# Optimization experiments

Hardware: AMD Instinct MI355X
Metric: run time of the kernel (lower is better)

Reference implementation:

```python
import jax, jax.numpy as jnp
import numpy as np

N_QUBITS = 16
N_LAYERS = 2
NUM_CLASSES = 10
BATCH = 256

# CNOT as (c_out, t_out, c_in, t_in)
_CNOT = np.zeros((2, 2, 2, 2), dtype=np.complex64)
_CNOT[0, 0, 0, 0] = 1; _CNOT[0, 1, 0, 1] = 1
_CNOT[1, 1, 1, 0] = 1; _CNOT[1, 0, 1, 1] = 1
CNOT = jnp.asarray(_CNOT)


def rot_matrix(phi, theta, omega):
    # PennyLane Rot = RZ(omega) @ RY(theta) @ RZ(phi)
    c, s = jnp.cos(theta / 2), jnp.sin(theta / 2)
    m00 = jnp.exp(-0.5j * (phi + omega)) * c
    m01 = -jnp.exp(0.5j * (phi - omega)) * s
    m10 = jnp.exp(-0.5j * (phi - omega)) * s
    m11 = jnp.exp(0.5j * (phi + omega)) * c
    return jnp.stack([jnp.stack([m00, m01]), jnp.stack([m10, m11])]).astype(jnp.complex64)


def apply_1q(state, U, w, n):
    # state: (B, 2**n); wire 0 = most-significant bit (PennyLane convention)
    B = state.shape[0]
    st = state.reshape(B, 2 ** w, 2, -1)
    st = jnp.einsum('oi,baic->baoc', U, st)
    return st.reshape(B, -1)


def apply_cnot(state, c, t, n):
    B = state.shape[0]
    st = state.reshape((B,) + (2,) * n)
    st = jnp.tensordot(CNOT, st, axes=[[2, 3], [c + 1, t + 1]])  # new c,t axes at front
    st = jnp.moveaxis(st, [0, 1], [c + 1, t + 1])
    return st.reshape(B, -1)


def circuit_expvals(x, q_params, n, n_layers):
    # AmplitudeEmbedding with normalize=True
    norm = jnp.sqrt(jnp.sum(x * x, axis=-1, keepdims=True))
    psi = (x / norm).astype(jnp.complex64)
    for l in range(n_layers):
        for w in range(n):
            U = rot_matrix(q_params[l, w, 0], q_params[l, w, 1], q_params[l, w, 2])
            psi = apply_1q(psi, U, w, n)
        r = (l % (n - 1)) + 1  # default StronglyEntanglingLayers ranges
        for w in range(n):
            psi = apply_cnot(psi, w, (w + r) % n, n)
    probs = psi.real ** 2 + psi.imag ** 2  # (B, 2**n)
    B = probs.shape[0]
    ev = []
    for w in range(n):
        p = probs.reshape(B, 2 ** w, 2, -1)
        ev.append(p[:, :, 0, :].sum(axis=(1, 2)) - p[:, :, 1, :].sum(axis=(1, 2)))
    return jnp.stack(ev, axis=1)  # (B, n)


def setup_inputs() -> dict:
    key = jax.random.key(0)
    k1, k2, k3, k4 = jax.random.split(key, 4)
    x = jax.random.normal(k1, (BATCH, 2 ** N_QUBITS), dtype=jnp.float32)
    q_params = jax.random.normal(k2, (N_LAYERS, N_QUBITS, 3), dtype=jnp.float32)
    lim = 1.0 / np.sqrt(N_QUBITS)
    W = jax.random.uniform(k3, (NUM_CLASSES, N_QUBITS), jnp.float32, -lim, lim)
    b = jax.random.uniform(k4, (NUM_CLASSES,), jnp.float32, -lim, lim)
    return {"x": x, "q_params": q_params, "W": W, "b": b}


def reference(x, q_params, W, b):
    feats = circuit_expvals(x, q_params, N_QUBITS, N_LAYERS)  # (B, n_qubits)
    return feats @ W.T + b
```

## Files before the change

kernel.cpp:

```cpp
#include <hip/hip_runtime.h>


#define BATCH 256
#define NCLS 10

typedef _Float16 h2 __attribute__((ext_vector_type(2)));
typedef float v2f __attribute__((ext_vector_type(2)));

#define KATTR __launch_bounds__(256, 4)

struct CircuitMeta { unsigned l1mask[16]; unsigned l1role[16]; unsigned fin[16]; };

__host__ __device__ constexpr CircuitMeta make_meta() {
  CircuitMeta m{};
  unsigned col[16] = {}, inv[16] = {};
  for (int w = 0; w < 16; ++w) { col[w] = 1u << (15 - w); inv[w] = 1u << (15 - w); }
  for (int w = 0; w < 16; ++w) { int c = w, t = (w + 1) & 15; col[c] ^= col[t]; inv[t] ^= inv[c]; }
  for (int w = 0; w < 16; ++w) { m.l1mask[w] = col[w]; m.l1role[w] = inv[w]; }
  for (int w = 0; w < 16; ++w) { int c = w, t = (w + 2) & 15; col[c] ^= col[t]; inv[t] ^= inv[c]; }
  for (int w = 0; w < 16; ++w) m.fin[w] = inv[w];
  return m;
}
constexpr CircuitMeta META = make_meta();

__host__ __device__ constexpr unsigned HASH(unsigned i) {
  return i ^ ((i >> 4) & 15u) ^ ((i >> 8) & 15u);
}

__device__ __forceinline__ h2 hfma(h2 a, h2 b, h2 c) {
  return __builtin_elementwise_fma(a, b, c);
}
__device__ __forceinline__ h2 hswp(h2 a) { return __builtin_shufflevector(a, a, 1, 0); }
__device__ __forceinline__ v2f vfma(v2f a, v2f b, v2f c) {
  return __builtin_elementwise_fma(a, b, c);
}
__device__ __forceinline__ unsigned U32(h2 a) { return __builtin_bit_cast(unsigned, a); }
__device__ __forceinline__ h2 H2(unsigned u) { return __builtin_bit_cast(h2, u); }
__device__ __forceinline__ unsigned AMPU(h2 r, h2 i, int l) {
  h2 a = l ? (h2){r.y, i.y} : (h2){r.x, i.x};
  return U32(a);
}

__device__ __forceinline__ float esel(int q, int pos, float e00, float e01,
                                      float e10, float e11) {
  int p = q ? 3 - pos : pos;
  return p == 0 ? e00 : p == 1 ? e01 : p == 2 ? e10 : e11;
}

template<int KB0,int KB1,int KB2,int KB3,int LB, unsigned MG, unsigned RG>
__device__ __forceinline__ void gateV(h2 (&Vr)[16], h2 (&Vi)[16],
                                      const float* __restrict__ g,
                                      int gi, unsigned tp) {
  constexpr unsigned cover = (1u<<KB0)|(1u<<KB1)|(1u<<KB2)|(1u<<KB3)|(1u<<LB);
  static_assert((MG & ~cover) == 0u, "gate mask not covered by stage reg bits");
  constexpr unsigned mk = ((MG>>KB0)&1u) | (((MG>>KB1)&1u)<<1)
                        | (((MG>>KB2)&1u)<<2) | (((MG>>KB3)&1u)<<3);
  constexpr int ml = (int)((MG>>LB)&1u);
  constexpr unsigned rk = ((RG>>KB0)&1u) | (((RG>>KB1)&1u)<<1)
                        | (((RG>>KB2)&1u)<<2) | (((RG>>KB3)&1u)<<3);
  constexpr int rl = (int)((RG>>LB)&1u);
  static_assert(mk != 0u || ml != 0, "empty mask");

  float u00r = g[gi*8+0], u00i = g[gi*8+1], u01r = g[gi*8+2], u01i = g[gi*8+3];
  float u10r = g[gi*8+4], u10i = g[gi*8+5], u11r = g[gi*8+6], u11i = g[gi*8+7];
  const bool s = (__popc(RG & tp) & 1) != 0;
  float e00r = s?u11r:u00r, e00i = s?u11i:u00i;
  float e01r = s?u10r:u01r, e01i = s?u10i:u01i;
  float e10r = s?u01r:u10r, e10i = s?u01i:u10i;
  float e11r = s?u00r:u11r, e11i = s?u00i:u11i;
  #define ER(q,pos) (_Float16)esel((q),(pos),e00r,e01r,e10r,e11r)
  #define EI(q,pos) (_Float16)esel((q),(pos),e00i,e01i,e10i,e11i)

  if constexpr (ml == 0) {
    static_assert((__builtin_popcount(rk & mk) & 1) == 1, "pair parity invariant");
    h2 c00r = {ER(0,0), ER(rl,0)}, c00i = {EI(0,0), EI(rl,0)};
    h2 c01r = {ER(0,1), ER(rl,1)}, c01i = {EI(0,1), EI(rl,1)};
    h2 c10r = {ER(0,2), ER(rl,2)}, c10i = {EI(0,2), EI(rl,2)};
    h2 c11r = {ER(0,3), ER(rl,3)}, c11i = {EI(0,3), EI(rl,3)};
    constexpr unsigned pivot = mk & (0u - mk);
    #pragma unroll
    for (int k0 = 0; k0 < 16; ++k0) {
      if (k0 & (int)pivot) continue;
      const int k1 = k0 ^ (int)mk;
      const bool podd = (__builtin_popcount(rk & (unsigned)k0) & 1) != 0;
      const h2 A0r = podd?c11r:c00r, A0i = podd?c11i:c00i;
      const h2 A1r = podd?c10r:c01r, A1i = podd?c10i:c01i;
      const h2 B0r = podd?c01r:c10r, B0i = podd?c01i:c10i;
      const h2 B1r = podd?c00r:c11r, B1i = podd?c00i:c11i;
      const h2 v0r = Vr[k0], v0i = Vi[k0], v1r = Vr[k1], v1i = Vi[k1];
      h2 n0r = A0r*v0r; n0r = hfma(-A0i, v0i, n0r);
      n0r = hfma(A1r, v1r, n0r); n0r = hfma(-A1i, v1i, n0r);
      h2 n0i = A0r*v0i; n0i = hfma(A0i, v0r, n0i);
      n0i = hfma(A1r, v1i, n0i); n0i = hfma(A1i, v1r, n0i);
      h2 n1r = B0r*v0r; n1r = hfma(-B0i, v0i, n1r);
      n1r = hfma(B1r, v1r, n1r); n1r = hfma(-B1i, v1i, n1r);
      h2 n1i = B0r*v0i; n1i = hfma(B0i, v0r, n1i);
      n1i = hfma(B1r, v1i, n1i); n1i = hfma(B1i, v1r, n1i);
      Vr[k0] = n0r; Vi[k0] = n0i; Vr[k1] = n1r; Vi[k1] = n1i;
    }
  } else if constexpr (mk == 0u) {
    static_assert(rl == 1, "lane-only gate requires rl==1");
    h2 CA0r = {ER(0,0), ER(1,0)}, CA0i = {EI(0,0), EI(1,0)};
    h2 CB0r = {ER(0,1), ER(1,1)}, CB0i = {EI(0,1), EI(1,1)};
    h2 CA1r = {ER(1,0), ER(0,0)}, CA1i = {EI(1,0), EI(0,0)};
    h2 CB1r = {ER(1,1), ER(0,1)}, CB1i = {EI(1,1), EI(0,1)};
    #pragma unroll
    for (int k = 0; k < 16; ++k) {
      const bool q = (__builtin_popcount(rk & (unsigned)k) & 1) != 0;
      const h2 CAr = q?CA1r:CA0r, CAi = q?CA1i:CA0i;
      const h2 CBr = q?CB1r:CB0r, CBi = q?CB1i:CB0i;
      const h2 vr = Vr[k], vi = Vi[k];
      const h2 svr = hswp(vr), svi = hswp(vi);
      h2 nr = CAr*vr; nr = hfma(-CAi, vi, nr);
      nr = hfma(CBr, svr, nr); nr = hfma(-CBi, svi, nr);
      h2 ni = CAr*vi; ni = hfma(CAi, vr, ni);
      ni = hfma(CBr, svi, ni); ni = hfma(CBi, svr, ni);
      Vr[k] = nr; Vi[k] = ni;
    }
  } else {
    constexpr int dm = __builtin_popcount(rk & mk) & 1;
    static_assert((dm ^ rl) == 1, "cross gate pair parity invariant");
    h2 CA0r = {ER(0,0), ER(rl,0)},          CA0i = {EI(0,0), EI(rl,0)};
    h2 CB0r = {ER(0,1), ER(rl,1)},          CB0i = {EI(0,1), EI(rl,1)};
    h2 CC0r = {ER(dm,0), ER(dm^rl,0)},      CC0i = {EI(dm,0), EI(dm^rl,0)};
    h2 CD0r = {ER(dm,1), ER(dm^rl,1)},      CD0i = {EI(dm,1), EI(dm^rl,1)};
    h2 CA1r = {ER(1,0), ER(1^rl,0)},        CA1i = {EI(1,0), EI(1^rl,0)};
    h2 CB1r = {ER(1,1), ER(1^rl,1)},        CB1i = {EI(1,1), EI(1^rl,1)};
    h2 CC1r = {ER(1^dm,0), ER(1^dm^rl,0)},  CC1i = {EI(1^dm,0), EI(1^dm^rl,0)};
    h2 CD1r = {ER(1^dm,1), ER(1^dm^rl,1)},  CD1i = {EI(1^dm,1), EI(1^dm^rl,1)};
    constexpr unsigned pivot = mk & (0u - mk);
    #pragma unroll
    for (int k0 = 0; k0 < 16; ++k0) {
      if (k0 & (int)pivot) continue;
      const int k1 = k0 ^ (int)mk;
      const bool q = (__builtin_popcount(rk & (unsigned)k0) & 1) != 0;
      const h2 CAr = q?CA1r:CA0r, CAi = q?CA1i:CA0i;
      const h2 CBr = q?CB1r:CB0r, CBi = q?CB1i:CB0i;
      const h2 CCr = q?CC1r:CC0r, CCi = q?CC1i:CC0i;
      const h2 CDr = q?CD1r:CD0r, CDi = q?CD1i:CD0i;
      const h2 vr = Vr[k0], vi = Vi[k0], ur = Vr[k1], ui = Vi[k1];
      const h2 sur = hswp(ur), sui = hswp(ui), svr = hswp(vr), svi = hswp(vi);
      h2 nvr = CAr*vr; nvr = hfma(-CAi, vi, nvr);
      nvr = hfma(CBr, sur, nvr); nvr = hfma(-CBi, sui, nvr);
      h2 nvi = CAr*vi; nvi = hfma(CAi, vr, nvi);
      nvi = hfma(CBr, sui, nvi); nvi = hfma(CBi, sur, nvi);
      h2 nur = CCr*ur; nur = hfma(-CCi, ui, nur);
      nur = hfma(CDr, svr, nur); nur = hfma(-CDi, svi, nur);
      h2 nui = CCr*ui; nui = hfma(CCi, ur, nui);
      nui = hfma(CDr, svi, nui); nui = hfma(CDi, svr, nui);
      Vr[k0] = nvr; Vi[k0] = nvi; Vr[k1] = nur; Vi[k1] = nui;
    }
  }
  #undef ER
  #undef EI
}

__global__ void prep_gates(const float* __restrict__ qp, float* __restrict__ g) {
  int i = threadIdx.x;
  if (i >= 32) return;
  float phi = qp[i*3+0], th = qp[i*3+1], om = qp[i*3+2];
  float cth = cosf(0.5f*th), sth = sinf(0.5f*th);
  float a = 0.5f*(phi+om), d = 0.5f*(phi-om);
  float ca = cosf(a), sa = sinf(a), cd = cosf(d), sd = sinf(d);
  g[i*8+0] =  ca*cth; g[i*8+1] = -sa*cth;
  g[i*8+2] = -cd*sth; g[i*8+3] = -sd*sth;
  g[i*8+4] =  cd*sth; g[i*8+5] = -sd*sth;
  g[i*8+6] =  ca*cth; g[i*8+7] =  sa*cth;
}

__global__ KATTR void passA(const float* __restrict__ x,
    unsigned* __restrict__ st, const float* __restrict__ g) {
  __shared__ unsigned L[8192];
  const int t = threadIdx.x;
  const int batch = blockIdx.x >> 3;
  const unsigned f = blockIdx.x & 7;
  const float* xb = x + ((size_t)batch << 16) + ((size_t)f << 13);

  h2 Vr[16], Vi[16];
  #pragma unroll
  for (int k = 0; k < 16; ++k) {
    Vr[k] = (h2){(_Float16)xb[((unsigned)k << 9) | (unsigned)t],
                 (_Float16)xb[((unsigned)k << 9) | 256u | (unsigned)t]};
    Vi[k] = (h2){(_Float16)0.f, (_Float16)0.f};
  }

  gateV<9,10,11,12,8, 0x1000u,0x1000u>(Vr, Vi, g, 3, 0u);
  gateV<9,10,11,12,8, 0x0800u,0x0800u>(Vr, Vi, g, 4, 0u);
  gateV<9,10,11,12,8, 0x0400u,0x0400u>(Vr, Vi, g, 5, 0u);
  gateV<9,10,11,12,8, 0x0200u,0x0200u>(Vr, Vi, g, 6, 0u);
  gateV<9,10,11,12,8, 0x0100u,0x0100u>(Vr, Vi, g, 7, 0u);

  {
    const unsigned wb = HASH((unsigned)t);
    #pragma unroll
    for (int k = 0; k < 16; ++k) {
      L[wb ^ HASH(((unsigned)k << 9))]        = AMPU(Vr[k], Vi[k], 0);
      L[wb ^ HASH(((unsigned)k << 9) | 256u)] = AMPU(Vr[k], Vi[k], 1);
    }
    __syncthreads();
    const unsigned rb = HASH((((unsigned)t & 0xF8u) << 5) | ((unsigned)t & 7u));
    #pragma unroll
    for (int k = 0; k < 16; ++k) {
      h2 h0 = H2(L[rb ^ HASH(((unsigned)k << 4))]);
      h2 h1 = H2(L[rb ^ HASH(((unsigned)k << 4) | 8u)]);
      Vr[k] = (h2){h0.x, h1.x};
      Vi[k] = (h2){h0.y, h1.y};
    }
  }

  gateV<4,5,6,7,3, 0x0080u,0x0080u>(Vr, Vi, g,  8, 0u);
  gateV<4,5,6,7,3, 0x0040u,0x0040u>(Vr, Vi, g,  9, 0u);
  gateV<4,5,6,7,3, 0x0020u,0x0020u>(Vr, Vi, g, 10, 0u);
  gateV<4,5,6,7,3, 0x0010u,0x0010u>(Vr, Vi, g, 11, 0u);
  gateV<4,5,6,7,3, 0x0008u,0x0008u>(Vr, Vi, g, 12, 0u);

  __syncthreads();
  {
    const unsigned wb = HASH((((unsigned)t & 0xF8u) << 5) | ((unsigned)t & 7u));
    #pragma unroll
    for (int k = 0; k < 16; ++k) {
      L[wb ^ HASH(((unsigned)k << 4))]      = AMPU(Vr[k], Vi[k], 0);
      L[wb ^ HASH(((unsigned)k << 4) | 8u)] = AMPU(Vr[k], Vi[k], 1);
    }
    __syncthreads();
    const unsigned rb = HASH((unsigned)t << 3);
    #pragma unroll
    for (int k = 0; k < 16; ++k) {
      const unsigned kv = ((unsigned)k & 7u) | (((unsigned)k & 8u) << 8);
      h2 h0 = H2(L[rb ^ HASH(kv)]);
      h2 h1 = H2(L[rb ^ HASH(kv | 4096u)]);
      Vr[k] = (h2){h0.x, h1.x};
      Vi[k] = (h2){h0.y, h1.y};
    }
  }

  gateV<0,1,2,11,12, 0x0004u,0x0004u>(Vr, Vi, g, 13, 0u);
  gateV<0,1,2,11,12, 0x0002u,0x0002u>(Vr, Vi, g, 14, 0u);
  gateV<0,1,2,11,12, 0x0001u,0x0001u>(Vr, Vi, g, 15, 0u);

  unsigned* outb = st + ((size_t)batch << 16) + ((size_t)f << 13);
  #pragma unroll
  for (int l = 0; l < 2; ++l) {
    #pragma unroll
    for (int kh = 0; kh < 2; ++kh) {
      uint4 q0, q1;
      q0.x = AMPU(Vr[kh*8+0], Vi[kh*8+0], l); q0.y = AMPU(Vr[kh*8+1], Vi[kh*8+1], l);
      q0.z = AMPU(Vr[kh*8+2], Vi[kh*8+2], l); q0.w = AMPU(Vr[kh*8+3], Vi[kh*8+3], l);
      q1.x = AMPU(Vr[kh*8+4], Vi[kh*8+4], l); q1.y = AMPU(Vr[kh*8+5], Vi[kh*8+5], l);
      q1.z = AMPU(Vr[kh*8+6], Vi[kh*8+6], l); q1.w = AMPU(Vr[kh*8+7], Vi[kh*8+7], l);
      const unsigned si = ((unsigned)l << 12) | ((unsigned)kh << 11) | ((unsigned)t << 3);
      *(uint4*)(outb + si) = q0;
      *(uint4*)(outb + si + 4) = q1;
    }
  }
}

__global__ KATTR void passB(unsigned* __restrict__ st,
    const float* __restrict__ g) {
  __shared__ unsigned L[8192];
  const int t = threadIdx.x;
  const int batch = blockIdx.x >> 3;
  const unsigned c = blockIdx.x & 7;
  unsigned* stb = st + ((size_t)batch << 16);

  const unsigned lbase = ((unsigned)t & 127u) | (((unsigned)t & 128u) << 3) | (c << 7);
  h2 Vr[16], Vi[16];
  #pragma unroll
  for (int k = 0; k < 16; ++k) {
    h2 h0 = H2(stb[((unsigned)k << 12) | lbase]);
    h2 h1 = H2(stb[((unsigned)k << 12) | 2048u | lbase]);
    Vr[k] = (h2){h0.x, h1.x};
    Vi[k] = (h2){h0.y, h1.y};
  }

  const unsigned tp1 = lbase;
  gateV<12,13,14,15,11, 0x8000u,0x8000u>(Vr, Vi, g, 0, tp1);
  gateV<12,13,14,15,11, 0x4000u,0x4000u>(Vr, Vi, g, 1, tp1);
  gateV<12,13,14,15,11, 0x2000u,0x2000u>(Vr, Vi, g, 2, tp1);
  gateV<12,13,14,15,11, META.l1mask[0], META.l1role[0]>(Vr, Vi, g, 16, tp1);
  gateV<12,13,14,15,11, META.l1mask[1], META.l1role[1]>(Vr, Vi, g, 17, tp1);
  gateV<12,13,14,15,11, META.l1mask[2], META.l1role[2]>(Vr, Vi, g, 18, tp1);
  gateV<12,13,14,15,11, META.l1mask[3], META.l1role[3]>(Vr, Vi, g, 19, tp1);

  {
    const unsigned wb = HASH((unsigned)t);
    #pragma unroll
    for (int k = 0; k < 16; ++k) {
      L[wb ^ HASH(((unsigned)k << 9))]        = AMPU(Vr[k], Vi[k], 0);
      L[wb ^ HASH(((unsigned)k << 9) | 256u)] = AMPU(Vr[k], Vi[k], 1);
    }
    __syncthreads();
    const unsigned rb = HASH((((unsigned)t & 0xF0u) << 5) | (((unsigned)t & 15u) << 1));
    #pragma unroll
    for (int k = 0; k < 16; ++k) {
      h2 h0 = H2(L[rb ^ HASH(((unsigned)k << 5))]);
      h2 h1 = H2(L[rb ^ HASH(((unsigned)k << 5) | 1u)]);
      Vr[k] = (h2){h0.x, h1.x};
      Vi[k] = (h2){h0.y, h1.y};
    }
  }

  const unsigned tp2 = (((unsigned)t & 0xF0u) << 8) | (((unsigned)t & 15u) << 1) | (c << 7);
  gateV<5,6,10,11,0, META.l1mask[4], META.l1role[4]>(Vr, Vi, g, 20, tp2);
  gateV<5,6,10,11,0, META.l1mask[9], META.l1role[9]>(Vr, Vi, g, 25, tp2);

  __syncthreads();
  {
    const unsigned wb = HASH((((unsigned)t & 0xF0u) << 5) | (((unsigned)t & 15u) << 1));
    #pragma unroll
    for (int k = 0; k < 16; ++k) {
      L[wb ^ HASH(((unsigned)k << 5))]      = AMPU(Vr[k], Vi[k], 0);
      L[wb ^ HASH(((unsigned)k << 5) | 1u)] = AMPU(Vr[k], Vi[k], 1);
    }
    __syncthreads();
    const unsigned rb = HASH((((unsigned)t & 0xFEu) << 5) | ((unsigned)t & 1u));
    #pragma unroll
    for (int k = 0; k < 16; ++k) {
      h2 h0 = H2(L[rb ^ HASH(((unsigned)k << 2))]);
      h2 h1 = H2(L[rb ^ HASH(((unsigned)k << 2) | 2u)]);
      Vr[k] = (h2){h0.x, h1.x};
      Vi[k] = (h2){h0.y, h1.y};
    }
  }

  const unsigned tp3 = (((unsigned)t & 0xFCu) << 8) | (((unsigned)t & 2u) << 5)
                     | ((unsigned)t & 1u) | (c << 7);
  gateV<2,3,4,5,1, META.l1mask[10], META.l1role[10]>(Vr, Vi, g, 26, tp3);
  gateV<2,3,4,5,1, META.l1mask[11], META.l1role[11]>(Vr, Vi, g, 27, tp3);
  gateV<2,3,4,5,1, META.l1mask[12], META.l1role[12]>(Vr, Vi, g, 28, tp3);
  gateV<2,3,4,5,1, META.l1mask[13], META.l1role[13]>(Vr, Vi, g, 29, tp3);

  __syncthreads();
  {
    const unsigned wb = HASH((((unsigned)t & 0xFEu) << 5) | ((unsigned)t & 1u));
    #pragma unroll
    for (int k = 0; k < 16; ++k) {
      L[wb ^ HASH(((unsigned)k << 2))]      = AMPU(Vr[k], Vi[k], 0);
      L[wb ^ HASH(((unsigned)k << 2) | 2u)] = AMPU(Vr[k], Vi[k], 1);
    }
    __syncthreads();
    const unsigned rb = HASH((unsigned)t << 2);
    #pragma unroll
    for (int k = 0; k < 16; ++k) {
      const unsigned kv = ((unsigned)k & 3u) | (((unsigned)k & 12u) << 9);
      h2 h0 = H2(L[rb ^ HASH(kv)]);
      h2 h1 = H2(L[rb ^ HASH(kv | 1024u)]);
      Vr[k] = (h2){h0.x, h1.x};
      Vi[k] = (h2){h0.y, h1.y};
    }
  }

  const unsigned tp4 = (((unsigned)t & 0xE0u) << 5) | (((unsigned)t & 31u) << 2) | (c << 7);
  gateV<0,1,14,15,13, META.l1mask[14], META.l1role[14]>(Vr, Vi, g, 30, tp4);
  gateV<0,1,14,15,13, META.l1mask[15], META.l1role[15]>(Vr, Vi, g, 31, tp4);

  #pragma unroll
  for (int l = 0; l < 2; ++l) {
    #pragma unroll
    for (int kh = 0; kh < 4; ++kh) {
      uint4 q;
      q.x = AMPU(Vr[kh*4+0], Vi[kh*4+0], l); q.y = AMPU(Vr[kh*4+1], Vi[kh*4+1], l);
      q.z = AMPU(Vr[kh*4+2], Vi[kh*4+2], l); q.w = AMPU(Vr[kh*4+3], Vi[kh*4+3], l);
      *(uint4*)(stb + (tp4 | ((unsigned)l << 13) | ((unsigned)kh << 14))) = q;
    }
  }
}

__global__ KATTR void passC(const unsigned* __restrict__ st,
    const float* __restrict__ g, float* __restrict__ partials) {
  __shared__ float R[4][17];
  const int t = threadIdx.x;
  const int batch = blockIdx.x >> 3;
  const unsigned f = blockIdx.x & 7;
  const unsigned* stb = st + ((size_t)batch << 16);

  const unsigned cbase = (f << 13) | (((unsigned)t & 192u) << 5) | ((unsigned)t & 63u);
  h2 Vr[16], Vi[16];
  #pragma unroll
  for (int k = 0; k < 16; ++k) {
    h2 h0 = H2(stb[cbase | ((unsigned)k << 7)]);
    h2 h1 = H2(stb[cbase | ((unsigned)k << 7) | 64u]);
    Vr[k] = (h2){h0.x, h1.x};
    Vi[k] = (h2){h0.y, h1.y};
  }

  gateV<7,8,9,10,6, META.l1mask[5], META.l1role[5]>(Vr, Vi, g, 21, cbase);
  gateV<7,8,9,10,6, META.l1mask[6], META.l1role[6]>(Vr, Vi, g, 22, cbase);
  gateV<7,8,9,10,6, META.l1mask[7], META.l1role[7]>(Vr, Vi, g, 23, cbase);
  gateV<7,8,9,10,6, META.l1mask[8], META.l1role[8]>(Vr, Vi, g, 24, cbase);

  v2f sv2[16], tot2 = (v2f){0.f, 0.f};
  #pragma unroll
  for (int w = 0; w < 16; ++w) sv2[w] = (v2f){0.f, 0.f};
  const v2f lm = (v2f){1.f, -1.f};
  #pragma unroll
  for (int k = 0; k < 16; ++k) {
    v2f vr = {(float)Vr[k].x, (float)Vr[k].y};
    v2f vi = {(float)Vi[k].x, (float)Vi[k].y};
    v2f pr = vfma(vi, vi, vr*vr);
    tot2 = tot2 + pr;
    v2f prm = pr * lm;
    #pragma unroll
    for (int w = 0; w < 16; ++w) {
      const unsigned m = META.fin[w];
      const bool fl = ((m >> 6) & 1u) != 0;
      const bool sk = (__builtin_popcount(m & ((unsigned)k << 7)) & 1) != 0;
      const v2f term = fl ? prm : pr;
      sv2[w] = sk ? (sv2[w] - term) : (sv2[w] + term);
    }
  }
  float sv[16];
  #pragma unroll
  for (int w = 0; w < 16; ++w) sv[w] = sv2[w].x + sv2[w].y;
  float tot = tot2.x + tot2.y;
  #pragma unroll
  for (int w = 0; w < 16; ++w)
    if (__popc(META.fin[w] & cbase) & 1) sv[w] = -sv[w];

  #pragma unroll
  for (int off = 32; off; off >>= 1) {
    tot += __shfl_xor(tot, off, 64);
    #pragma unroll
    for (int w = 0; w < 16; ++w) sv[w] += __shfl_xor(sv[w], off, 64);
  }
  const int wave = t >> 6, lane = t & 63;
  if (lane == 0) {
    #pragma unroll
    for (int w = 0; w < 16; ++w) R[wave][w] = sv[w];
    R[wave][16] = tot;
  }
  __syncthreads();
  if (t < 17) {
    const float s2 = R[0][t] + R[1][t] + R[2][t] + R[3][t];
    partials[(size_t)blockIdx.x * 17 + t] = s2;
  }
}

__global__ __launch_bounds__(64) void head(const float* __restrict__ partials,
    const float* __restrict__ W, const float* __restrict__ bias,
    float* __restrict__ out) {
  const int b = blockIdx.x, tid = threadIdx.x;
  __shared__ float red[17];
  __shared__ float ev[16];
  if (tid < 17) {
    float s = 0.f;
    #pragma unroll
    for (int ch = 0; ch < 8; ++ch) s += partials[(size_t)((b << 3) + ch) * 17 + tid];
    red[tid] = s;
  }
  __syncthreads();
  if (tid < 16) ev[tid] = red[tid] / red[16];
  __syncthreads();
  if (tid < NCLS) {
    float o = bias[tid];
    #pragma unroll
    for (int w = 0; w < 16; ++w) o += ev[w] * W[tid*16 + w];
    out[b*NCLS + tid] = o;
  }
}

extern "C" void kernel_launch(void* const* d_in, const int* in_sizes, int n_in,
                              void* d_out, int out_size, void* d_ws, size_t ws_size,
                              hipStream_t stream) {
  const float* x  = (const float*)d_in[0];
  const float* qp = (const float*)d_in[1];
  const float* W  = (const float*)d_in[2];
  const float* bv = (const float*)d_in[3];
  float* out = (float*)d_out;

  unsigned* st     = (unsigned*)d_ws;
  float*    gates  = (float*)((char*)d_ws + (size_t)BATCH * 65536 * 4);
  float*    parts  = (float*)((char*)gates + 1024);

  prep_gates<<<dim3(1), dim3(64), 0, stream>>>(qp, gates);
  passA<<<dim3(BATCH*8), dim3(256), 0, stream>>>(x, st, gates);
  passB<<<dim3(BATCH*8), dim3(256), 0, stream>>>(st, gates);
  passC<<<dim3(BATCH*8), dim3(256), 0, stream>>>(st, gates, parts);
  head<<<dim3(BATCH), dim3(64), 0, stream>>>(parts, W, bv, out);
}
```

Baseline: 190.4 us.

## Halve shared memory by splitting LDS transposes into two half-phases

Shrinks the LDS staging buffer in passA and passB from 8192 to 4096 words. Each register-to-shared-memory transpose now runs in two rounds, with half the data or half the threads per round and extra barriers plus temporary registers in between. Halving per-block LDS is meant to let more blocks reside per CU and raise occupancy. In exchange it doubles the barriers, adds register pressure from the tA temporaries, and makes the code more intricate.

```diff
diff --git a/kernel.cpp b/kernel.cpp
--- a/kernel.cpp
+++ b/kernel.cpp
@@ -25,6 +25,10 @@
 
 __host__ __device__ constexpr unsigned HASH(unsigned i) {
   return i ^ ((i >> 4) & 15u) ^ ((i >> 8) & 15u);
+}
+__host__ __device__ constexpr unsigned D5H(unsigned i) {
+  unsigned h = HASH(i);
+  return (h & 31u) | ((h >> 6) << 5);
 }
 
 __device__ __forceinline__ h2 hfma(h2 a, h2 b, h2 c) {
@@ -170,7 +174,7 @@
 
 __global__ KATTR void passA(const float* __restrict__ x,
     unsigned* __restrict__ st, const float* __restrict__ g) {
-  __shared__ unsigned L[8192];
+  __shared__ unsigned L[4096];
   const int t = threadIdx.x;
   const int batch = blockIdx.x >> 3;
   const unsigned f = blockIdx.x & 7;
@@ -193,18 +197,39 @@
   {
     const unsigned wb = HASH((unsigned)t);
     #pragma unroll
-    for (int k = 0; k < 16; ++k) {
-      L[wb ^ HASH(((unsigned)k << 9))]        = AMPU(Vr[k], Vi[k], 0);
+    for (int k = 0; k < 8; ++k) {
+      L[wb ^ HASH((unsigned)k << 9)]          = AMPU(Vr[k], Vi[k], 0);
       L[wb ^ HASH(((unsigned)k << 9) | 256u)] = AMPU(Vr[k], Vi[k], 1);
     }
     __syncthreads();
-    const unsigned rb = HASH((((unsigned)t & 0xF8u) << 5) | ((unsigned)t & 7u));
-    #pragma unroll
-    for (int k = 0; k < 16; ++k) {
-      h2 h0 = H2(L[rb ^ HASH(((unsigned)k << 4))]);
-      h2 h1 = H2(L[rb ^ HASH(((unsigned)k << 4) | 8u)]);
-      Vr[k] = (h2){h0.x, h1.x};
-      Vi[k] = (h2){h0.y, h1.y};
+    h2 tA[16];
+    const unsigned rb = HASH((((unsigned)t & 0x78u) << 5) | ((unsigned)t & 7u));
+    if ((t & 128) == 0) {
+      #pragma unroll
+      for (int k = 0; k < 16; ++k) {
+        h2 h0 = H2(L[rb ^ HASH((unsigned)k << 4)]);
+        h2 h1 = H2(L[rb ^ HASH(((unsigned)k << 4) | 8u)]);
+        if (k < 8) { Vr[k] = (h2){h0.x, h1.x}; Vi[k] = (h2){h0.y, h1.y}; }
+        else       { tA[k - 8] = (h2){h0.x, h1.x}; tA[k] = (h2){h0.y, h1.y}; }
+      }
+    }
+    __syncthreads();
+    #pragma unroll
+    for (int k = 8; k < 16; ++k) {
+      L[wb ^ HASH((unsigned)(k & 7) << 9)]          = AMPU(Vr[k], Vi[k], 0);
+      L[wb ^ HASH(((unsigned)(k & 7) << 9) | 256u)] = AMPU(Vr[k], Vi[k], 1);
+    }
+    __syncthreads();
+    if ((t & 128) != 0) {
+      #pragma unroll
+      for (int k = 0; k < 16; ++k) {
+        h2 h0 = H2(L[rb ^ HASH((unsigned)k << 4)]);
+        h2 h1 = H2(L[rb ^ HASH(((unsigned)k << 4) | 8u)]);
+        Vr[k] = (h2){h0.x, h1.x}; Vi[k] = (h2){h0.y, h1.y};
+      }
+    } else {
+      #pragma unroll
+      for (int k = 8; k < 16; ++k) { Vr[k] = tA[k - 8]; Vi[k] = tA[k]; }
     }
   }
 
@@ -216,21 +241,37 @@
 
   __syncthreads();
   {
-    const unsigned wb = HASH((((unsigned)t & 0xF8u) << 5) | ((unsigned)t & 7u));
-    #pragma unroll
-    for (int k = 0; k < 16; ++k) {
-      L[wb ^ HASH(((unsigned)k << 4))]      = AMPU(Vr[k], Vi[k], 0);
-      L[wb ^ HASH(((unsigned)k << 4) | 8u)] = AMPU(Vr[k], Vi[k], 1);
-    }
-    __syncthreads();
+    const unsigned wb = HASH((((unsigned)t & 0x78u) << 5) | ((unsigned)t & 7u));
+    if ((t & 128) == 0) {
+      #pragma unroll
+      for (int k = 0; k < 16; ++k) {
+        L[wb ^ HASH((unsigned)k << 4)]        = AMPU(Vr[k], Vi[k], 0);
+        L[wb ^ HASH(((unsigned)k << 4) | 8u)] = AMPU(Vr[k], Vi[k], 1);
+      }
+    }
+    __syncthreads();
+    h2 tA[16];
     const unsigned rb = HASH((unsigned)t << 3);
     #pragma unroll
     for (int k = 0; k < 16; ++k) {
       const unsigned kv = ((unsigned)k & 7u) | (((unsigned)k & 8u) << 8);
-      h2 h0 = H2(L[rb ^ HASH(kv)]);
-      h2 h1 = H2(L[rb ^ HASH(kv | 4096u)]);
-      Vr[k] = (h2){h0.x, h1.x};
-      Vi[k] = (h2){h0.y, h1.y};
+      tA[k] = H2(L[rb ^ HASH(kv)]);
+    }
+    __syncthreads();
+    if ((t & 128) != 0) {
+      #pragma unroll
+      for (int k = 0; k < 16; ++k) {
+        L[wb ^ HASH((unsigned)k << 4)]        = AMPU(Vr[k], Vi[k], 0);
+        L[wb ^ HASH(((unsigned)k << 4) | 8u)] = AMPU(Vr[k], Vi[k], 1);
+      }
+    }
+    __syncthreads();
+    #pragma unroll
+    for (int k = 0; k < 16; ++k) {
+      const unsigned kv = ((unsigned)k & 7u) | (((unsigned)k & 8u) << 8);
+      h2 h1 = H2(L[rb ^ HASH(kv)]);
+      Vr[k] = (h2){tA[k].x, h1.x};
+      Vi[k] = (h2){tA[k].y, h1.y};
     }
   }
 
@@ -257,7 +298,7 @@
 
 __global__ KATTR void passB(unsigned* __restrict__ st,
     const float* __restrict__ g) {
-  __shared__ unsigned L[8192];
+  __shared__ unsigned L[4096];
   const int t = threadIdx.x;
   const int batch = blockIdx.x >> 3;
   const unsigned c = blockIdx.x & 7;
@@ -285,18 +326,39 @@
   {
     const unsigned wb = HASH((unsigned)t);
     #pragma unroll
-    for (int k = 0; k < 16; ++k) {
-      L[wb ^ HASH(((unsigned)k << 9))]        = AMPU(Vr[k], Vi[k], 0);
+    for (int k = 0; k < 8; ++k) {
+      L[wb ^ HASH((unsigned)k << 9)]          = AMPU(Vr[k], Vi[k], 0);
       L[wb ^ HASH(((unsigned)k << 9) | 256u)] = AMPU(Vr[k], Vi[k], 1);
     }
     __syncthreads();
-    const unsigned rb = HASH((((unsigned)t & 0xF0u) << 5) | (((unsigned)t & 15u) << 1));
-    #pragma unroll
-    for (int k = 0; k < 16; ++k) {
-      h2 h0 = H2(L[rb ^ HASH(((unsigned)k << 5))]);
-      h2 h1 = H2(L[rb ^ HASH(((unsigned)k << 5) | 1u)]);
-      Vr[k] = (h2){h0.x, h1.x};
-      Vi[k] = (h2){h0.y, h1.y};
+    h2 tA[16];
+    const unsigned rb = HASH((((unsigned)t & 0x70u) << 5) | (((unsigned)t & 15u) << 1));
+    if ((t & 128) == 0) {
+      #pragma unroll
+      for (int k = 0; k < 16; ++k) {
+        h2 h0 = H2(L[rb ^ HASH((unsigned)k << 5)]);
+        h2 h1 = H2(L[rb ^ HASH(((unsigned)k << 5) | 1u)]);
+        if (k < 8) { Vr[k] = (h2){h0.x, h1.x}; Vi[k] = (h2){h0.y, h1.y}; }
+        else       { tA[k - 8] = (h2){h0.x, h1.x}; tA[k] = (h2){h0.y, h1.y}; }
+      }
+    }
+    __syncthreads();
+    #pragma unroll
+    for (int k = 8; k < 16; ++k) {
+      L[wb ^ HASH((unsigned)(k & 7) << 9)]          = AMPU(Vr[k], Vi[k], 0);
+      L[wb ^ HASH(((unsigned)(k & 7) << 9) | 256u)] = AMPU(Vr[k], Vi[k], 1);
+    }
+    __syncthreads();
+    if ((t & 128) != 0) {
+      #pragma unroll
+      for (int k = 0; k < 16; ++k) {
+        h2 h0 = H2(L[rb ^ HASH((unsigned)k << 5)]);
+        h2 h1 = H2(L[rb ^ HASH(((unsigned)k << 5) | 1u)]);
+        Vr[k] = (h2){h0.x, h1.x}; Vi[k] = (h2){h0.y, h1.y};
+      }
+    } else {
+      #pragma unroll
+      for (int k = 8; k < 16; ++k) { Vr[k] = tA[k - 8]; Vi[k] = tA[k]; }
     }
   }
 
@@ -306,21 +368,41 @@
 
   __syncthreads();
   {
-    const unsigned wb = HASH((((unsigned)t & 0xF0u) << 5) | (((unsigned)t & 15u) << 1));
-    #pragma unroll
-    for (int k = 0; k < 16; ++k) {
-      L[wb ^ HASH(((unsigned)k << 5))]      = AMPU(Vr[k], Vi[k], 0);
-      L[wb ^ HASH(((unsigned)k << 5) | 1u)] = AMPU(Vr[k], Vi[k], 1);
-    }
-    __syncthreads();
-    const unsigned rb = HASH((((unsigned)t & 0xFEu) << 5) | ((unsigned)t & 1u));
-    #pragma unroll
-    for (int k = 0; k < 16; ++k) {
-      h2 h0 = H2(L[rb ^ HASH(((unsigned)k << 2))]);
-      h2 h1 = H2(L[rb ^ HASH(((unsigned)k << 2) | 2u)]);
-      Vr[k] = (h2){h0.x, h1.x};
-      Vi[k] = (h2){h0.y, h1.y};
-    }
+    unsigned hw = HASH((((unsigned)t & 0xF0u) << 5) | (((unsigned)t & 15u) << 1));
+    const unsigned wb = (hw & 31u) | ((hw >> 6) << 5);
+    #pragma unroll
+    for (int kk = 0; kk < 8; ++kk) {
+      const int k = 2 * kk;
+      L[wb ^ D5H((unsigned)k << 5)]        = AMPU(Vr[k], Vi[k], 0);
+      L[wb ^ D5H(((unsigned)k << 5) | 1u)] = AMPU(Vr[k], Vi[k], 1);
+    }
+    __syncthreads();
+    unsigned hr = HASH((((unsigned)t & 0xFEu) << 5) | ((unsigned)t & 1u));
+    const unsigned rb = (hr & 31u) | ((hr >> 6) << 5);
+    h2 tA[8];
+    #pragma unroll
+    for (int k = 0; k < 8; ++k) {
+      h2 h0 = H2(L[rb ^ D5H((unsigned)k << 2)]);
+      h2 h1 = H2(L[rb ^ D5H(((unsigned)k << 2) | 2u)]);
+      if ((k & 1) == 0) { Vr[k] = (h2){h0.x, h1.x}; Vi[k] = (h2){h0.y, h1.y}; }
+      else { tA[k >> 1] = (h2){h0.x, h1.x}; tA[4 + (k >> 1)] = (h2){h0.y, h1.y}; }
+    }
+    __syncthreads();
+    #pragma unroll
+    for (int kk = 0; kk < 8; ++kk) {
+      const int k = 2 * kk + 1;
+      L[wb ^ D5H((unsigned)k << 5)]        = AMPU(Vr[k], Vi[k], 0);
+      L[wb ^ D5H(((unsigned)k << 5) | 1u)] = AMPU(Vr[k], Vi[k], 1);
+    }
+    __syncthreads();
+    #pragma unroll
+    for (int k = 8; k < 16; ++k) {
+      h2 h0 = H2(L[rb ^ D5H((unsigned)k << 2)]);
+      h2 h1 = H2(L[rb ^ D5H(((unsigned)k << 2) | 2u)]);
+      Vr[k] = (h2){h0.x, h1.x}; Vi[k] = (h2){h0.y, h1.y};
+    }
+    #pragma unroll
+    for (int j = 0; j < 4; ++j) { Vr[2*j+1] = tA[j]; Vi[2*j+1] = tA[4+j]; }
   }
 
   const unsigned tp3 = (((unsigned)t & 0xFCu) << 8) | (((unsigned)t & 2u) << 5)
@@ -332,21 +414,44 @@
 
   __syncthreads();
   {
-    const unsigned wb = HASH((((unsigned)t & 0xFEu) << 5) | ((unsigned)t & 1u));
-    #pragma unroll
-    for (int k = 0; k < 16; ++k) {
-      L[wb ^ HASH(((unsigned)k << 2))]      = AMPU(Vr[k], Vi[k], 0);
-      L[wb ^ HASH(((unsigned)k << 2) | 2u)] = AMPU(Vr[k], Vi[k], 1);
-    }
-    __syncthreads();
+    const unsigned wb = HASH((((unsigned)t & 0x7Eu) << 5) | ((unsigned)t & 1u));
+    if ((t & 128) == 0) {
+      #pragma unroll
+      for (int k = 0; k < 16; ++k) {
+        L[wb ^ HASH((unsigned)k << 2)]        = AMPU(Vr[k], Vi[k], 0);
+        L[wb ^ HASH(((unsigned)k << 2) | 2u)] = AMPU(Vr[k], Vi[k], 1);
+      }
+    }
+    __syncthreads();
+    h2 tA[16];
     const unsigned rb = HASH((unsigned)t << 2);
     #pragma unroll
-    for (int k = 0; k < 16; ++k) {
-      const unsigned kv = ((unsigned)k & 3u) | (((unsigned)k & 12u) << 9);
+    for (int k = 0; k < 8; ++k) {
+      const unsigned kv = ((unsigned)k & 3u) | (((unsigned)k & 4u) << 9);
       h2 h0 = H2(L[rb ^ HASH(kv)]);
       h2 h1 = H2(L[rb ^ HASH(kv | 1024u)]);
-      Vr[k] = (h2){h0.x, h1.x};
-      Vi[k] = (h2){h0.y, h1.y};
+      if ((t & 128) == 0) { Vr[k] = (h2){h0.x, h1.x}; Vi[k] = (h2){h0.y, h1.y}; }
+      else { tA[k] = (h2){h0.x, h1.x}; tA[8 + k] = (h2){h0.y, h1.y}; }
+    }
+    __syncthreads();
+    if ((t & 128) != 0) {
+      #pragma unroll
+      for (int k = 0; k < 16; ++k) {
+        L[wb ^ HASH((unsigned)k << 2)]        = AMPU(Vr[k], Vi[k], 0);
+        L[wb ^ HASH(((unsigned)k << 2) | 2u)] = AMPU(Vr[k], Vi[k], 1);
+      }
+    }
+    __syncthreads();
+    #pragma unroll
+    for (int k = 8; k < 16; ++k) {
+      const unsigned kv = ((unsigned)k & 3u) | (((unsigned)k & 4u) << 9);
+      h2 h0 = H2(L[rb ^ HASH(kv)]);
+      h2 h1 = H2(L[rb ^ HASH(kv | 1024u)]);
+      Vr[k] = (h2){h0.x, h1.x}; Vi[k] = (h2){h0.y, h1.y};
+    }
+    if ((t & 128) != 0) {
+      #pragma unroll
+      for (int k = 0; k < 8; ++k) { Vr[k] = tA[k]; Vi[k] = tA[8 + k]; }
     }
   }
 
```

After: 192.0 us. About the same (+0.8%).
